# Kernel optimization log

Hardware: AMD Instinct MI355X
Metric: run time of the kernel (lower is better)

Reference implementation:

```python
import jax, jax.numpy as jnp
import numpy as np
import math

B, S, D, H, L, F = 32, 512, 512, 8, 4, 1024
TD = 4 * D  # time embedding dim
DH = D // H
SCALE = 1.0 / math.sqrt(DH)


def _ln(x, g, b):
    m = jnp.mean(x, -1, keepdims=True)
    v = jnp.var(x, -1, keepdims=True)
    return (x - m) * jax.lax.rsqrt(v + 1e-5) * g + b


def setup_inputs() -> dict:
    key = jax.random.key(0)
    ks = jax.random.split(key, 12)
    w = lambda k, shp: jax.random.normal(k, shp, dtype=jnp.float32) * 0.02
    return {
        "x": jax.random.normal(ks[0], (B, S, D), dtype=jnp.float32),
        "time": jax.random.uniform(ks[1], (B,), dtype=jnp.float32) * 1000.0,
        "time_w1": w(ks[2], (TD, D)), "time_b1": jnp.zeros((TD,), jnp.float32),
        "time_w2": w(ks[3], (TD, TD)), "time_b2": jnp.zeros((TD,), jnp.float32),
        "Wq": w(ks[4], (L, D, D)), "bq": jnp.zeros((L, D), jnp.float32),
        "Wk": w(ks[5], (L, D, D)), "bk": jnp.zeros((L, D), jnp.float32),
        "Wv": w(ks[6], (L, D, D)), "bv": jnp.zeros((L, D), jnp.float32),
        "Wo": w(ks[7], (L, D, D)), "bo": jnp.zeros((L, D), jnp.float32),
        "attn_g": jnp.ones((L, D), jnp.float32), "attn_b": jnp.zeros((L, D), jnp.float32),
        "ffn_g": jnp.ones((L, D), jnp.float32), "ffn_b": jnp.zeros((L, D), jnp.float32),
        "W1": w(ks[8], (L, 2 * F, D)), "b1": jnp.zeros((L, 2 * F), jnp.float32),
        "W2": w(ks[9], (L, D, F)), "b2": jnp.zeros((L, D), jnp.float32),
        "Wt": w(ks[10], (L, 4 * F, TD)), "bt": jnp.zeros((L, 4 * F), jnp.float32),
        "head_g": jnp.ones((D,), jnp.float32), "head_b": jnp.zeros((D,), jnp.float32),
        "Wh": w(ks[11], (D, D)), "bh": jnp.zeros((D,), jnp.float32),
    }


def _forward(x, time, time_w1, time_b1, time_w2, time_b2,
             Wq, bq, Wk, bk, Wv, bv, Wo, bo,
             attn_g, attn_b, ffn_g, ffn_b,
             W1, b1, W2, b2, Wt, bt,
             head_g, head_b, Wh, bh):
    Bsz = x.shape[0]
    # --- sinusoidal time embedding + time MLP ---
    half = D // 2
    freqs = jnp.exp(jnp.arange(half, dtype=jnp.float32) * (-math.log(10000.0) / (half - 1)))
    e = time[:, None] * freqs[None, :]
    temb = jnp.concatenate([jnp.sin(e), jnp.cos(e)], axis=-1)  # [B, D]
    temb = jax.nn.gelu(temb @ time_w1.T + time_b1, approximate=False) @ time_w2.T + time_b2  # [B, 4D]
    for i in range(L):
        # attention (prenorm; block 0 skips the norm since first_prenormalization=False)
        h = x if i == 0 else _ln(x, attn_g[i], attn_b[i])
        q = (h @ Wq[i].T + bq[i]).reshape(Bsz, S, H, DH)
        k = (h @ Wk[i].T + bk[i]).reshape(Bsz, S, H, DH)
        v = (h @ Wv[i].T + bv[i]).reshape(Bsz, S, H, DH)
        logits = jnp.einsum('bqhd,bkhd->bhqk', q, k) * SCALE
        probs = jax.nn.softmax(logits, axis=-1)
        o = jnp.einsum('bhqk,bkhd->bqhd', probs, v).reshape(Bsz, S, D)
        x = x + (o @ Wo[i].T + bo[i])
        # FFN with FiLM time conditioning and ReGLU activation
        h = _ln(x, ffn_g[i], ffn_b[i])
        h1 = h @ W1[i].T + b1[i]  # [B, S, 2F]
        tm = jax.nn.silu(temb) @ Wt[i].T + bt[i]  # [B, 4F]
        scale, shift = jnp.split(tm[:, None, :], 2, axis=-1)  # each [B, 1, 2F]
        h1 = h1 * (scale + 1.0) + shift
        a, g = jnp.split(h1, 2, axis=-1)  # ReGLU: a * relu(g)
        x = x + ((a * jax.nn.relu(g)) @ W2[i].T + b2[i])
    # head: last token -> LayerNorm -> ReLU -> Linear
    z = _ln(x[:, -1], head_g, head_b)
    return jax.nn.relu(z) @ Wh.T + bh


def reference(x, time, time_w1, time_b1, time_w2, time_b2,
              Wq, bq, Wk, bk, Wv, bv, Wo, bo,
              attn_g, attn_b, ffn_g, ffn_b,
              W1, b1, W2, b2, Wt, bt,
              head_g, head_b, Wh, bh):
    return _forward(x, time, time_w1, time_b1, time_w2, time_b2,
                    Wq, bq, Wk, bk, Wv, bv, Wo, bo,
                    attn_g, attn_b, ffn_g, ffn_b,
                    W1, b1, W2, b2, Wt, bt,
                    head_g, head_b, Wh, bh)
```

## Files before the change

kernel.cpp:

```cpp
#include <hip/hip_runtime.h>
#include <math.h>

typedef __bf16 bf16_t;
typedef __bf16 bf16x8 __attribute__((ext_vector_type(8)));
typedef float f32x4 __attribute__((ext_vector_type(4)));

__device__ __forceinline__ void gload_lds16(const void* g, void* l) {
    __builtin_amdgcn_global_load_lds(
        (const __attribute__((address_space(1))) void*)g,
        (__attribute__((address_space(3))) void*)l, 16, 0, 0);
}

__global__ void k_f2b(const float* __restrict__ in, bf16_t* __restrict__ out, int n8) {
    int idx = blockIdx.x * 256 + threadIdx.x;
    if (idx >= n8) return;
    const float* p = in + (size_t)idx * 8;
    bf16x8 r;
#pragma unroll
    for (int j = 0; j < 8; j++) r[j] = (bf16_t)p[j];
    *(bf16x8*)(out + (size_t)idx * 8) = r;
}

__global__ void k_f2b_s(const float* __restrict__ in, bf16_t* __restrict__ out,
                        int seg8, int dstride8) {
    int idx = blockIdx.x * 256 + threadIdx.x;
    int seg = idx / seg8, rem = idx - seg * seg8;
    const float* p = in + (size_t)idx * 8;
    bf16x8 r;
#pragma unroll
    for (int j = 0; j < 8; j++) r[j] = (bf16_t)p[j];
    *(bf16x8*)(out + ((size_t)seg * dstride8 + rem) * 8) = r;
}

__global__ void k_time_embed(const float* __restrict__ time, float* __restrict__ temb0) {
    int b = blockIdx.x;
    int j = threadIdx.x;
    float f = __expf((float)j * -0.036118981458730134f);
    float e = time[b] * f;
    temb0[(size_t)b * 512 + j] = sinf(e);
    temb0[(size_t)b * 512 + 256 + j] = cosf(e);
}

template<bool DO_NORM, bool IN32>
__global__ void k_ln(const void* __restrict__ xp, const float* __restrict__ g,
                     const float* __restrict__ b, bf16_t* __restrict__ out) {
    int row = blockIdx.x * 4 + (threadIdx.x >> 6);
    int lane = threadIdx.x & 63;
    float vals[8];
    if (IN32) {
        const float* xr = (const float*)xp + (size_t)row * 512 + lane * 8;
        float4 v0 = *(const float4*)xr;
        float4 v1 = *(const float4*)(xr + 4);
        vals[0] = v0.x; vals[1] = v0.y; vals[2] = v0.z; vals[3] = v0.w;
        vals[4] = v1.x; vals[5] = v1.y; vals[6] = v1.z; vals[7] = v1.w;
    } else {
        bf16x8 xv = *(const bf16x8*)((const bf16_t*)xp + (size_t)row * 512 + lane * 8);
#pragma unroll
        for (int j = 0; j < 8; j++) vals[j] = (float)xv[j];
    }
    bf16x8 r;
    if (DO_NORM) {
        float s = 0.f, sq = 0.f;
#pragma unroll
        for (int j = 0; j < 8; j++) { s += vals[j]; sq += vals[j] * vals[j]; }
#pragma unroll
        for (int m = 1; m < 64; m <<= 1) { s += __shfl_xor(s, m, 64); sq += __shfl_xor(sq, m, 64); }
        float mean = s * (1.0f / 512.0f);
        float var = sq * (1.0f / 512.0f) - mean * mean;
        float rstd = rsqrtf(var + 1e-5f);
        float4 g0 = *(const float4*)(g + lane * 8);
        float4 g1 = *(const float4*)(g + lane * 8 + 4);
        float4 b0 = *(const float4*)(b + lane * 8);
        float4 b1 = *(const float4*)(b + lane * 8 + 4);
        float gs[8] = {g0.x, g0.y, g0.z, g0.w, g1.x, g1.y, g1.z, g1.w};
        float bs[8] = {b0.x, b0.y, b0.z, b0.w, b1.x, b1.y, b1.z, b1.w};
#pragma unroll
        for (int j = 0; j < 8; j++) r[j] = (bf16_t)((vals[j] - mean) * rstd * gs[j] + bs[j]);
    } else {
#pragma unroll
        for (int j = 0; j < 8; j++) r[j] = (bf16_t)vals[j];
    }
    *(bf16x8*)(out + (size_t)row * 512 + lane * 8) = r;
}

__global__ void k_head_prep(const bf16_t* __restrict__ x, const float* __restrict__ g,
                            const float* __restrict__ b, float* __restrict__ z) {
    int row = blockIdx.x * 4 + (threadIdx.x >> 6);
    int lane = threadIdx.x & 63;
    bf16x8 xv = *(const bf16x8*)(x + ((size_t)row * 512 + 511) * 512 + lane * 8);
    float vals[8];
#pragma unroll
    for (int j = 0; j < 8; j++) vals[j] = (float)xv[j];
    float s = 0.f, sq = 0.f;
#pragma unroll
    for (int j = 0; j < 8; j++) { s += vals[j]; sq += vals[j] * vals[j]; }
#pragma unroll
    for (int m = 1; m < 64; m <<= 1) { s += __shfl_xor(s, m, 64); sq += __shfl_xor(sq, m, 64); }
    float mean = s * (1.0f / 512.0f);
    float var = sq * (1.0f / 512.0f) - mean * mean;
    float rstd = rsqrtf(var + 1e-5f);
    float o[8];
#pragma unroll
    for (int j = 0; j < 8; j++) {
        float gv = g[lane * 8 + j], bv = b[lane * 8 + j];
        o[j] = fmaxf((vals[j] - mean) * rstd * gv + bv, 0.0f);
    }
    float* zr = z + (size_t)row * 512 + lane * 8;
    *(float4*)zr = make_float4(o[0], o[1], o[2], o[3]);
    *(float4*)(zr + 4) = make_float4(o[4], o[5], o[6], o[7]);
}

template<int ACT, int K, bool OUTB>
__global__ __launch_bounds__(256, 2)
void k_gemm_tm(const float* __restrict__ A, const float* __restrict__ W,
               const float* __restrict__ bias, void* __restrict__ outp, int N) {
    __shared__ float Asm[32][516];
    const int t = threadIdx.x;
    const int kq = t & 7, rw = (t >> 3) & 7, bh = t >> 6;
    const int n0 = blockIdx.x * 32;
    float acc[4][8] = {};
    for (int k0 = 0; k0 < K; k0 += 512) {
        __syncthreads();
#pragma unroll
        for (int i = 0; i < 16; i++) {
            int fid = t + i * 256;
            int row = fid >> 7, cc = (fid & 127) << 2;
            *(float4*)&Asm[row][cc] = *(const float4*)&A[(size_t)row * K + k0 + cc];
        }
        __syncthreads();
#pragma unroll 4
        for (int j = 0; j < 16; j++) {
            int kk = kq * 4 + j * 32;
            float4 w4[4];
#pragma unroll
            for (int r = 0; r < 4; r++)
                w4[r] = *(const float4*)&W[(size_t)(n0 + rw + r * 8) * K + k0 + kk];
#pragma unroll
            for (int b = 0; b < 8; b++) {
                float4 a4 = *(const float4*)&Asm[bh * 8 + b][kk];
#pragma unroll
                for (int r = 0; r < 4; r++)
                    acc[r][b] += a4.x * w4[r].x + a4.y * w4[r].y + a4.z * w4[r].z + a4.w * w4[r].w;
            }
        }
    }
#pragma unroll
    for (int m = 1; m < 8; m <<= 1)
#pragma unroll
        for (int r = 0; r < 4; r++)
#pragma unroll
            for (int b = 0; b < 8; b++)
                acc[r][b] += __shfl_xor(acc[r][b], m, 64);
    if (kq == 0) {
#pragma unroll
        for (int r = 0; r < 4; r++) {
            int n = n0 + rw + r * 8;
            float bv = bias[n];
#pragma unroll
            for (int b = 0; b < 8; b++) {
                float v = acc[r][b] + bv;
                if (ACT == 1) v = 0.5f * v * (1.0f + erff(v * 0.70710678118654752f));
                if (ACT == 2) v = v / (1.0f + __expf(-v));
                if (OUTB) ((bf16_t*)outp)[(size_t)(bh * 8 + b) * N + n] = (bf16_t)v;
                else      ((float*)outp)[(size_t)(bh * 8 + b) * N + n] = v;
            }
        }
    }
}

__global__ void k_fill_tmt(const float* __restrict__ bt, float* __restrict__ dst) {
    int i = blockIdx.x * 256 + threadIdx.x;
    dst[i] = bt[i >> 5];
}

__global__ void k_silu_t(const float* __restrict__ tmp, bf16_t* __restrict__ t2s_b) {
    int i = blockIdx.x * 256 + threadIdx.x;
    float v = tmp[i];
    v = v / (1.0f + __expf(-v));
    int n = i >> 5, b = i & 31;
    t2s_b[(size_t)b * 2048 + n] = (bf16_t)v;
}

__global__ __launch_bounds__(256, 4)
void k_gemm_wt(const float* __restrict__ Wf, const bf16_t* __restrict__ Bb16,
               float* __restrict__ dst) {
    __shared__ __align__(16) bf16_t Abuf[64 * 64];
    __shared__ __align__(16) bf16_t Bbuf[32 * 64];
    const int tid = threadIdx.x;
    const int m0 = blockIdx.x * 64;
    const int k0 = blockIdx.y * 512;
    const int lane = tid & 63, wave = tid >> 6;
    const int arow = tid >> 2, aseg = tid & 3;
    const int brow = tid >> 3, bseg = tid & 7;
    const int aswz = (arow & 7) << 4;
    const char* Bg = (const char*)Bb16 + (size_t)brow * 4096 + ((bseg * 16) ^ ((brow & 7) << 4));
    char* BbL = (char*)Bbuf + tid * 16;
    const float* Ar0 = Wf + (size_t)(m0 + arow) * 2048 + k0 + aseg * 16;
    f32x4 acc[2] = {};
    for (int kk0 = 0; kk0 < 512; kk0 += 64) {
        float4 a4[4];
#pragma unroll
        for (int i = 0; i < 4; i++) a4[i] = *(const float4*)(Ar0 + kk0 + i * 4);
        __syncthreads();
        gload_lds16(Bg + (size_t)(k0 + kk0) * 2, BbL);
        bf16x8 c0, c1;
#pragma unroll
        for (int i = 0; i < 4; i++) {
            const float* af = (const float*)&a4[i];
#pragma unroll
            for (int j = 0; j < 4; j++) {
                if (i < 2) c0[i * 4 + j] = (bf16_t)af[j];
                else       c1[(i - 2) * 4 + j] = (bf16_t)af[j];
            }
        }
        int base = arow * 128 + aseg * 32;
        *(bf16x8*)((char*)Abuf + (base ^ aswz)) = c0;
        *(bf16x8*)((char*)Abuf + ((base + 16) ^ aswz)) = c1;
        __syncthreads();
#pragma unroll
        for (int kk = 0; kk < 2; kk++) {
            int ar = wave * 16 + (lane & 15);
            bf16x8 af = *(const bf16x8*)((const char*)Abuf + ar * 128 +
                        ((kk * 64 + (lane >> 4) * 16) ^ ((ar & 7) << 4)));
#pragma unroll
            for (int j = 0; j < 2; j++) {
                int br = j * 16 + (lane & 15);
                bf16x8 bfr = *(const bf16x8*)((const char*)Bbuf + br * 128 +
                             ((kk * 64 + (lane >> 4) * 16) ^ ((br & 7) << 4)));
                acc[j] = __builtin_amdgcn_mfma_f32_16x16x32_bf16(af, bfr, acc[j], 0, 0, 0);
            }
        }
    }
#pragma unroll
    for (int j = 0; j < 2; j++)
#pragma unroll
        for (int r = 0; r < 4; r++) {
            int mrow = m0 + wave * 16 + (lane >> 4) * 4 + r;
            atomicAdd(&dst[(size_t)mrow * 32 + j * 16 + (lane & 15)], acc[j][r]);
        }
}

enum { EPI_QKV = 0, EPI_RESID = 1, EPI_FILMGLU = 2 };

template<int EPI, int K, int NBY, int BM, bool RS32>
__global__ __launch_bounds__(BM * 2, 4)
void k_gemm_bt(const bf16_t* __restrict__ A, const bf16_t* __restrict__ W,
               const float* __restrict__ bias, const float* __restrict__ bias2,
               const float* __restrict__ bias3,
               void* __restrict__ out0, const void* __restrict__ rsp, void* __restrict__ out2,
               const float* __restrict__ tm) {
    constexpr int T   = BM * 2;
    constexpr int RPR = BM / 4;
    constexpr int BR  = 512 / BM;
    __shared__ __align__(16) bf16_t Abuf[BM * 64];
    __shared__ __align__(16) bf16_t Bbuf[128 * 64];
    const int tid = threadIdx.x;
    const int cpx = gridDim.x >> 3;
    const int wg = (blockIdx.x & 7) * cpx + (blockIdx.x >> 3);
    const int bx = wg / NBY;
    const int by = wg - bx * NBY;
    const int m0 = bx * BM;
    const int lane = tid & 63;
    const int wid = tid >> 6;
    const int wrM = (wid >> 1) * 64;
    const int wN  = wid & 1;
    const int wc  = wN * 64;

    const int srow = tid >> 3;
    const int goff = ((tid & 7) * 16) ^ ((srow & 7) << 4);
    const char* Ag = (const char*)A;
    const char* Wg = (const char*)W;
    char* AbL = (char*)Abuf + tid * 16;
    char* BbL = (char*)Bbuf + tid * 16;
    int growB[BR];
#pragma unroll
    for (int i = 0; i < BR; i++) {
        int r = srow + i * RPR;
        if (EPI == EPI_FILMGLU) {
            int half = (r >> 5) & 1;
            int base = by * 64 + (r >> 6) * 32 + (r & 31);
            growB[i] = half * 1024 + base;
        } else {
            growB[i] = by * 128 + r;
        }
    }

    f32x4 acc[4][4] = {};
    for (int k0 = 0; k0 < K * 2; k0 += 128) {
        __syncthreads();
#pragma unroll
        for (int i = 0; i < 4; i++)
            gload_lds16(Ag + (size_t)(m0 + srow + i * RPR) * (K * 2) + k0 + goff, AbL + i * (T * 16));
#pragma unroll
        for (int i = 0; i < BR; i++)
            gload_lds16(Wg + (size_t)growB[i] * (K * 2) + k0 + goff, BbL + i * (T * 16));
        __syncthreads();
#pragma unroll
        for (int kk = 0; kk < 2; kk++) {
            bf16x8 af[4], bfr[4];
#pragma unroll
            for (int i = 0; i < 4; i++) {
                int ar = wrM + i * 16 + (lane & 15);
                af[i] = *(const bf16x8*)((const char*)Abuf + ar * 128 +
                         ((kk * 64 + (lane >> 4) * 16) ^ ((ar & 7) << 4)));
                int br = wc + i * 16 + (lane & 15);
                bfr[i] = *(const bf16x8*)((const char*)Bbuf + br * 128 +
                         ((kk * 64 + (lane >> 4) * 16) ^ ((br & 7) << 4)));
            }
#pragma unroll
            for (int i = 0; i < 4; i++)
#pragma unroll
                for (int j = 0; j < 4; j++)
                    acc[i][j] = __builtin_amdgcn_mfma_f32_16x16x32_bf16(af[i], bfr[j], acc[i][j], 0, 0, 0);
        }
    }

    const int b = m0 >> 9;
    if (EPI == EPI_QKV) {
        const int which = by >> 2;
        bf16_t* op = (bf16_t*)(which == 0 ? out0 : which == 1 ? (void*)rsp : out2);
        const float* bp = which == 0 ? bias : which == 1 ? bias2 : bias3;
#pragma unroll
        for (int i = 0; i < 4; i++) {
#pragma unroll
            for (int r = 0; r < 4; r++) {
                int s = (m0 + wrM + i * 16 + (lane >> 4) * 4 + r) & 511;
#pragma unroll
                for (int j = 0; j < 4; j++) {
                    int c = (by & 3) * 128 + wc + j * 16 + (lane & 15);
                    float v = acc[i][j][r] + bp[c];
                    int h = c >> 6, dh = c & 63;
                    op[(((size_t)b * 8 + h) * 512 + s) * 64 + dh] = (bf16_t)v;
                }
            }
        }
    } else if (EPI == EPI_RESID) {
        bf16_t* op = (bf16_t*)out0;
#pragma unroll
        for (int i = 0; i < 4; i++) {
#pragma unroll
            for (int r = 0; r < 4; r++) {
                int row = m0 + wrM + i * 16 + (lane >> 4) * 4 + r;
#pragma unroll
                for (int j = 0; j < 4; j++) {
                    int col = by * 128 + wc + j * 16 + (lane & 15);
                    size_t idx = (size_t)row * 512 + col;
                    float rsv = RS32 ? ((const float*)rsp)[idx] : (float)((const bf16_t*)rsp)[idx];
                    op[idx] = (bf16_t)(rsv + acc[i][j][r] + bias[col]);
                }
            }
        }
    } else {
        bf16_t* op = (bf16_t*)out0;
#pragma unroll
        for (int i = 0; i < 4; i++) {
#pragma unroll
            for (int r = 0; r < 4; r++) {
                int row = m0 + wrM + i * 16 + (lane >> 4) * 4 + r;
#pragma unroll
                for (int jj = 0; jj < 2; jj++) {
                    int colA = by * 64 + wN * 32 + jj * 16 + (lane & 15);
                    float av = acc[i][jj][r] + bias[colA];
                    float gv = acc[i][jj + 2][r] + bias[1024 + colA];
                    float sa = tm[(size_t)colA * 32 + b];
                    float ha = tm[(size_t)(2048 + colA) * 32 + b];
                    float sg = tm[(size_t)(1024 + colA) * 32 + b];
                    float hg = tm[(size_t)(3072 + colA) * 32 + b];
                    av = av * (1.0f + sa) + ha;
                    gv = gv * (1.0f + sg) + hg;
                    op[(size_t)row * 1024 + colA] = (bf16_t)(av * fmaxf(gv, 0.0f));
                }
            }
        }
    }
}

__global__ __launch_bounds__(256, 2)
void k_attn(const bf16_t* __restrict__ q, const bf16_t* __restrict__ k,
            const bf16_t* __restrict__ v, bf16_t* __restrict__ o) {
    __shared__ bf16_t q_lds[2][64][72];
    __shared__ bf16_t k_lds[64][72];
    __shared__ bf16_t vt_lds[64 * 72];
    __shared__ bf16_t p_lds[64][72];
    const int tid = threadIdx.x;
    const int lane = tid & 63;
    const int wave = tid >> 6;
    const int cpx = gridDim.x >> 3;
    const int wg = ((int)blockIdx.x & 7) * cpx + ((int)blockIdx.x >> 3);
    const int bh = wg >> 2;
    const int qt2 = wg & 3;
    const bf16_t* kb = k + (size_t)bh * 512 * 64;
    const bf16_t* vb = v + (size_t)bh * 512 * 64;
    const int sr = tid >> 2;
    const int sc = (tid & 3) * 16;
#pragma unroll
    for (int qi = 0; qi < 2; qi++) {
        const bf16_t* qb = q + ((size_t)bh * 512 + qt2 * 128 + qi * 64) * 64;
        bf16x8 a0 = *(const bf16x8*)(qb + sr * 64 + sc);
        bf16x8 a1 = *(const bf16x8*)(qb + sr * 64 + sc + 8);
        bf16x8 ra, rb;
#pragma unroll
        for (int j = 0; j < 8; j++) {
            ra[j] = (bf16_t)((float)a0[j] * 0.125f);
            rb[j] = (bf16_t)((float)a1[j] * 0.125f);
        }
        *(bf16x8*)&q_lds[qi][sr][sc] = ra;
        *(bf16x8*)&q_lds[qi][sr][sc + 8] = rb;
    }
    bf16x8 kr0, kr1, vr0, vr1;
    {
        const bf16_t* ks = kb + (size_t)sr * 64 + sc;
        const bf16_t* vs = vb + (size_t)sr * 64 + sc;
        kr0 = *(const bf16x8*)ks; kr1 = *(const bf16x8*)(ks + 8);
        vr0 = *(const bf16x8*)vs; vr1 = *(const bf16x8*)(vs + 8);
    }
    float mrow[2][4], lrow[2][4];
    f32x4 oacc[2][4] = {};
#pragma unroll
    for (int qi = 0; qi < 2; qi++)
#pragma unroll
        for (int r = 0; r < 4; r++) { mrow[qi][r] = -1e30f; lrow[qi][r] = 0.f; }
    const int swz0 = ((sc >> 3) & 7) << 4;
    const int swz1 = (((sc + 8) >> 3) & 7) << 4;
    for (int kt = 0; kt < 8; kt++) {
        __syncthreads();
        {
            *(bf16x8*)&k_lds[sr][sc] = kr0;
            *(bf16x8*)&k_lds[sr][sc + 8] = kr1;
            char* vbase = (char*)vt_lds;
            int so0 = (sr * 2) ^ swz0;
            int so1 = (sr * 2) ^ swz1;
#pragma unroll
            for (int j = 0; j < 8; j++) {
                *(bf16_t*)(vbase + (sc + j) * 144 + so0) = vr0[j];
                *(bf16_t*)(vbase + (sc + 8 + j) * 144 + so1) = vr1[j];
            }
        }
        __syncthreads();
        if (kt < 7) {
            const bf16_t* ks = kb + ((size_t)(kt + 1) * 64 + sr) * 64 + sc;
            const bf16_t* vs = vb + ((size_t)(kt + 1) * 64 + sr) * 64 + sc;
            kr0 = *(const bf16x8*)ks; kr1 = *(const bf16x8*)(ks + 8);
            vr0 = *(const bf16x8*)vs; vr1 = *(const bf16x8*)(vs + 8);
        }
#pragma unroll
        for (int qi = 0; qi < 2; qi++) {
            f32x4 sacc[4] = {};
#pragma unroll
            for (int kk = 0; kk < 2; kk++) {
                bf16x8 aq = *(const bf16x8*)&q_lds[qi][wave * 16 + (lane & 15)][kk * 32 + (lane >> 4) * 8];
#pragma unroll
                for (int c = 0; c < 4; c++) {
                    bf16x8 bk8 = *(const bf16x8*)&k_lds[c * 16 + (lane & 15)][kk * 32 + (lane >> 4) * 8];
                    sacc[c] = __builtin_amdgcn_mfma_f32_16x16x32_bf16(aq, bk8, sacc[c], 0, 0, 0);
                }
            }
#pragma unroll
            for (int r = 0; r < 4; r++) {
                float mx = fmaxf(fmaxf(sacc[0][r], sacc[1][r]), fmaxf(sacc[2][r], sacc[3][r]));
#pragma unroll
                for (int m = 1; m < 16; m <<= 1) mx = fmaxf(mx, __shfl_xor(mx, m, 64));
                float newm = fmaxf(mrow[qi][r], mx);
                float fsc = __expf(mrow[qi][r] - newm);
                mrow[qi][r] = newm;
                float p0 = __expf(sacc[0][r] - newm);
                float p1 = __expf(sacc[1][r] - newm);
                float p2 = __expf(sacc[2][r] - newm);
                float p3 = __expf(sacc[3][r] - newm);
                float ps = p0 + p1 + p2 + p3;
#pragma unroll
                for (int m = 1; m < 16; m <<= 1) ps += __shfl_xor(ps, m, 64);
                lrow[qi][r] = lrow[qi][r] * fsc + ps;
#pragma unroll
                for (int c = 0; c < 4; c++) oacc[qi][c][r] *= fsc;
                int qrow = wave * 16 + (lane >> 4) * 4 + r;
                p_lds[qrow][(lane & 15)] = (bf16_t)p0;
                p_lds[qrow][16 + (lane & 15)] = (bf16_t)p1;
                p_lds[qrow][32 + (lane & 15)] = (bf16_t)p2;
                p_lds[qrow][48 + (lane & 15)] = (bf16_t)p3;
            }
#pragma unroll
            for (int kk = 0; kk < 2; kk++) {
                bf16x8 ap = *(const bf16x8*)&p_lds[wave * 16 + (lane & 15)][kk * 32 + (lane >> 4) * 8];
#pragma unroll
                for (int c = 0; c < 4; c++) {
                    int d0 = c * 16 + (lane & 15);
                    int xo = ((d0 >> 3) & 7) << 4;
                    bf16x8 bv8 = *(const bf16x8*)((const char*)vt_lds + d0 * 144 +
                                  ((kk * 64 + (lane >> 4) * 16) ^ xo));
                    oacc[qi][c] = __builtin_amdgcn_mfma_f32_16x16x32_bf16(ap, bv8, oacc[qi][c], 0, 0, 0);
                }
            }
        }
    }
    const int b = bh >> 3, h = bh & 7;
#pragma unroll
    for (int qi = 0; qi < 2; qi++) {
#pragma unroll
        for (int r = 0; r < 4; r++) {
            int s = qt2 * 128 + qi * 64 + wave * 16 + (lane >> 4) * 4 + r;
            float inv = 1.0f / lrow[qi][r];
#pragma unroll
            for (int c = 0; c < 4; c++) {
                o[((size_t)b * 512 + s) * 512 + h * 64 + c * 16 + (lane & 15)] = (bf16_t)(oacc[qi][c][r] * inv);
            }
        }
    }
}

extern "C" void kernel_launch(void* const* d_in, const int* in_sizes, int n_in,
                              void* d_out, int out_size, void* d_ws, size_t ws_size,
                              hipStream_t stream) {
    const float* x_in   = (const float*)d_in[0];
    const float* time_in= (const float*)d_in[1];
    const float* tw1    = (const float*)d_in[2];
    const float* tb1    = (const float*)d_in[3];
    const float* tw2    = (const float*)d_in[4];
    const float* tb2    = (const float*)d_in[5];
    const float* Wq     = (const float*)d_in[6];
    const float* bq     = (const float*)d_in[7];
    const float* Wk     = (const float*)d_in[8];
    const float* bk     = (const float*)d_in[9];
    const float* Wv     = (const float*)d_in[10];
    const float* bv     = (const float*)d_in[11];
    const float* Wo     = (const float*)d_in[12];
    const float* bo     = (const float*)d_in[13];
    const float* attn_g = (const float*)d_in[14];
    const float* attn_b = (const float*)d_in[15];
    const float* ffn_g  = (const float*)d_in[16];
    const float* ffn_b  = (const float*)d_in[17];
    const float* W1     = (const float*)d_in[18];
    const float* b1     = (const float*)d_in[19];
    const float* W2     = (const float*)d_in[20];
    const float* b2     = (const float*)d_in[21];
    const float* Wt     = (const float*)d_in[22];
    const float* bt     = (const float*)d_in[23];
    const float* head_g = (const float*)d_in[24];
    const float* head_b = (const float*)d_in[25];
    const float* Wh     = (const float*)d_in[26];
    const float* bh     = (const float*)d_in[27];

    size_t off = 0;
    auto alloc = [&](size_t bytes) {
        void* r = (char*)d_ws + off;
        off += (bytes + 255) & ~(size_t)255;
        return r;
    };
    bf16_t* wqkv_b = (bf16_t*)alloc((size_t)4 * 3 * 512 * 512 * 2);
    bf16_t* wo_b   = (bf16_t*)alloc((size_t)4 * 512 * 512 * 2);
    bf16_t* w1_b   = (bf16_t*)alloc((size_t)4 * 2048 * 512 * 2);
    bf16_t* w2_b   = (bf16_t*)alloc((size_t)4 * 512 * 1024 * 2);
    bf16_t* x_ws   = (bf16_t*)alloc((size_t)16384 * 512 * 2);
    bf16_t* h_b    = (bf16_t*)alloc((size_t)16384 * 512 * 2);
    bf16_t* q_b    = (bf16_t*)alloc((size_t)16384 * 512 * 2);
    bf16_t* k_b    = (bf16_t*)alloc((size_t)16384 * 512 * 2);
    bf16_t* v_b    = (bf16_t*)alloc((size_t)16384 * 512 * 2);
    bf16_t* o_b    = (bf16_t*)alloc((size_t)16384 * 512 * 2);
    bf16_t* act_b  = (bf16_t*)alloc((size_t)16384 * 1024 * 2);
    float*  temb0  = (float*)alloc((size_t)32 * 512 * 4);
    bf16_t* t1_b   = (bf16_t*)alloc((size_t)32 * 2048 * 2);
    float*  tmp2   = (float*)alloc((size_t)2048 * 32 * 4);
    bf16_t* t2s_b  = (bf16_t*)alloc((size_t)32 * 2048 * 2);
    float*  tm_t   = (float*)alloc((size_t)16384 * 32 * 4);
    float*  z      = (float*)alloc((size_t)32 * 512 * 4);

    k_f2b_s<<<512, 256, 0, stream>>>(Wq, wqkv_b,          32768, 98304);
    k_f2b_s<<<512, 256, 0, stream>>>(Wk, wqkv_b + 262144, 32768, 98304);
    k_f2b_s<<<512, 256, 0, stream>>>(Wv, wqkv_b + 524288, 32768, 98304);
    k_f2b<<<512, 256, 0, stream>>>(Wo, wo_b, 131072);
    k_f2b<<<2048, 256, 0, stream>>>(W1, w1_b, 524288);
    k_f2b<<<1024, 256, 0, stream>>>(W2, w2_b, 262144);

    k_time_embed<<<32, 256, 0, stream>>>(time_in, temb0);
    k_gemm_tm<1, 512, true><<<64, 256, 0, stream>>>(temb0, tw1, tb1, t1_b, 2048);
    k_fill_tmt<<<256, 256, 0, stream>>>(tb2, tmp2);
    k_gemm_wt<<<dim3(32, 4), 256, 0, stream>>>(tw2, t1_b, tmp2);
    k_silu_t<<<256, 256, 0, stream>>>(tmp2, t2s_b);
    k_fill_tmt<<<2048, 256, 0, stream>>>(bt, tm_t);
    k_gemm_wt<<<dim3(256, 4), 256, 0, stream>>>(Wt, t2s_b, tm_t);

    for (int l = 0; l < 4; l++) {
        if (l == 0)
            k_ln<false, true><<<4096, 256, 0, stream>>>(x_in, nullptr, nullptr, h_b);
        else
            k_ln<true, false><<<4096, 256, 0, stream>>>(x_ws, attn_g + l * 512, attn_b + l * 512, h_b);

        k_gemm_bt<EPI_QKV, 512, 12, 128, false><<<1536, 256, 0, stream>>>(
            h_b, wqkv_b + (size_t)l * 786432,
            bq + l * 512, bk + l * 512, bv + l * 512,
            q_b, k_b, v_b, nullptr);

        k_attn<<<1024, 256, 0, stream>>>(q_b, k_b, v_b, o_b);

        if (l == 0)
            k_gemm_bt<EPI_RESID, 512, 4, 128, true><<<512, 256, 0, stream>>>(
                o_b, wo_b + (size_t)l * 262144,
                bo + l * 512, nullptr, nullptr,
                x_ws, x_in, nullptr, nullptr);
        else
            k_gemm_bt<EPI_RESID, 512, 4, 128, false><<<512, 256, 0, stream>>>(
                o_b, wo_b + (size_t)l * 262144,
                bo + l * 512, nullptr, nullptr,
                x_ws, x_ws, nullptr, nullptr);

        k_ln<true, false><<<4096, 256, 0, stream>>>(x_ws, ffn_g + l * 512, ffn_b + l * 512, h_b);

        k_gemm_bt<EPI_FILMGLU, 512, 16, 128, false><<<2048, 256, 0, stream>>>(
            h_b, w1_b + (size_t)l * 1048576,
            b1 + l * 2048, nullptr, nullptr,
            act_b, nullptr, nullptr, tm_t + (size_t)l * 4096 * 32);

        k_gemm_bt<EPI_RESID, 1024, 4, 128, false><<<512, 256, 0, stream>>>(
            act_b, w2_b + (size_t)l * 524288,
            b2 + l * 512, nullptr, nullptr,
            x_ws, x_ws, nullptr, nullptr);
    }

    k_head_prep<<<8, 256, 0, stream>>>(x_ws, head_g, head_b, z);
    k_gemm_tm<0, 512, false><<<16, 256, 0, stream>>>(z, Wh, bh, (float*)d_out, 512);
}
```

Baseline: 1.075 ms.

## Emit V transposed from QKV GEMM and simplify attention V staging

The QKV projection GEMM now computes the V block with swapped MFMA operands and writes V in a [b,h,dh,s] transposed layout. The attention kernel can then stage V into LDS with vector stores instead of per-element scattered transposing writes. It also folds log2(e) into the Q scale so softmax uses exp2f, raises the occupancy hint to 3 blocks per SM, and adds s_setprio around the MFMA sections. The transposed epilogue writes scattered 2-byte stores along s, which may make the GEMM's store pattern less efficient.

```diff
diff --git a/kernel.cpp b/kernel.cpp
--- a/kernel.cpp
+++ b/kernel.cpp
@@ -265,6 +265,7 @@
     const int wrM = (wid >> 1) * 64;
     const int wN  = wid & 1;
     const int wc  = wN * 64;
+    const bool vtr = (EPI == EPI_QKV) && ((by >> 2) == 2);
 
     const int srow = tid >> 3;
     const int goff = ((tid & 7) * 16) ^ ((srow & 7) << 4);
@@ -307,11 +308,19 @@
                 bfr[i] = *(const bf16x8*)((const char*)Bbuf + br * 128 +
                          ((kk * 64 + (lane >> 4) * 16) ^ ((br & 7) << 4)));
             }
-#pragma unroll
-            for (int i = 0; i < 4; i++)
-#pragma unroll
-                for (int j = 0; j < 4; j++)
-                    acc[i][j] = __builtin_amdgcn_mfma_f32_16x16x32_bf16(af[i], bfr[j], acc[i][j], 0, 0, 0);
+            if (vtr) {
+#pragma unroll
+                for (int i = 0; i < 4; i++)
+#pragma unroll
+                    for (int j = 0; j < 4; j++)
+                        acc[i][j] = __builtin_amdgcn_mfma_f32_16x16x32_bf16(bfr[j], af[i], acc[i][j], 0, 0, 0);
+            } else {
+#pragma unroll
+                for (int i = 0; i < 4; i++)
+#pragma unroll
+                    for (int j = 0; j < 4; j++)
+                        acc[i][j] = __builtin_amdgcn_mfma_f32_16x16x32_bf16(af[i], bfr[j], acc[i][j], 0, 0, 0);
+            }
         }
     }
 
@@ -320,17 +329,33 @@
         const int which = by >> 2;
         bf16_t* op = (bf16_t*)(which == 0 ? out0 : which == 1 ? (void*)rsp : out2);
         const float* bp = which == 0 ? bias : which == 1 ? bias2 : bias3;
-#pragma unroll
-        for (int i = 0; i < 4; i++) {
-#pragma unroll
-            for (int r = 0; r < 4; r++) {
-                int s = (m0 + wrM + i * 16 + (lane >> 4) * 4 + r) & 511;
-#pragma unroll
-                for (int j = 0; j < 4; j++) {
-                    int c = (by & 3) * 128 + wc + j * 16 + (lane & 15);
-                    float v = acc[i][j][r] + bp[c];
-                    int h = c >> 6, dh = c & 63;
-                    op[(((size_t)b * 8 + h) * 512 + s) * 64 + dh] = (bf16_t)v;
+        if (vtr) {
+#pragma unroll
+            for (int i = 0; i < 4; i++) {
+#pragma unroll
+                for (int r = 0; r < 4; r++) {
+#pragma unroll
+                    for (int j = 0; j < 4; j++) {
+                        int c = (by & 3) * 128 + wc + j * 16 + (lane >> 4) * 4 + r;
+                        int s = (m0 + wrM + i * 16 + (lane & 15)) & 511;
+                        float v = acc[i][j][r] + bp[c];
+                        op[(((size_t)b * 8 + (c >> 6)) * 64 + (c & 63)) * 512 + s] = (bf16_t)v;
+                    }
+                }
+            }
+        } else {
+#pragma unroll
+            for (int i = 0; i < 4; i++) {
+#pragma unroll
+                for (int r = 0; r < 4; r++) {
+                    int s = (m0 + wrM + i * 16 + (lane >> 4) * 4 + r) & 511;
+#pragma unroll
+                    for (int j = 0; j < 4; j++) {
+                        int c = (by & 3) * 128 + wc + j * 16 + (lane & 15);
+                        float v = acc[i][j][r] + bp[c];
+                        int h = c >> 6, dh = c & 63;
+                        op[(((size_t)b * 8 + h) * 512 + s) * 64 + dh] = (bf16_t)v;
+                    }
                 }
             }
         }
@@ -375,12 +400,12 @@
     }
 }
 
-__global__ __launch_bounds__(256, 2)
+__global__ __launch_bounds__(256, 3)
 void k_attn(const bf16_t* __restrict__ q, const bf16_t* __restrict__ k,
-            const bf16_t* __restrict__ v, bf16_t* __restrict__ o) {
+            const bf16_t* __restrict__ vt, bf16_t* __restrict__ o) {
     __shared__ bf16_t q_lds[2][64][72];
     __shared__ bf16_t k_lds[64][72];
-    __shared__ bf16_t vt_lds[64 * 72];
+    __shared__ bf16_t vt_lds[64][72];
     __shared__ bf16_t p_lds[64][72];
     const int tid = threadIdx.x;
     const int lane = tid & 63;
@@ -390,9 +415,10 @@
     const int bh = wg >> 2;
     const int qt2 = wg & 3;
     const bf16_t* kb = k + (size_t)bh * 512 * 64;
-    const bf16_t* vb = v + (size_t)bh * 512 * 64;
+    const bf16_t* vb = vt + (size_t)bh * 64 * 512;
     const int sr = tid >> 2;
     const int sc = (tid & 3) * 16;
+    const float QS = 0.125f * 1.44269504088896340736f;
 #pragma unroll
     for (int qi = 0; qi < 2; qi++) {
         const bf16_t* qb = q + ((size_t)bh * 512 + qt2 * 128 + qi * 64) * 64;
@@ -401,8 +427,8 @@
         bf16x8 ra, rb;
 #pragma unroll
         for (int j = 0; j < 8; j++) {
-            ra[j] = (bf16_t)((float)a0[j] * 0.125f);
-            rb[j] = (bf16_t)((float)a1[j] * 0.125f);
+            ra[j] = (bf16_t)((float)a0[j] * QS);
+            rb[j] = (bf16_t)((float)a1[j] * QS);
         }
         *(bf16x8*)&q_lds[qi][sr][sc] = ra;
         *(bf16x8*)&q_lds[qi][sr][sc + 8] = rb;
@@ -410,7 +436,7 @@
     bf16x8 kr0, kr1, vr0, vr1;
     {
         const bf16_t* ks = kb + (size_t)sr * 64 + sc;
-        const bf16_t* vs = vb + (size_t)sr * 64 + sc;
+        const bf16_t* vs = vb + (size_t)sr * 512 + sc;
         kr0 = *(const bf16x8*)ks; kr1 = *(const bf16x8*)(ks + 8);
         vr0 = *(const bf16x8*)vs; vr1 = *(const bf16x8*)(vs + 8);
     }
@@ -420,32 +446,25 @@
     for (int qi = 0; qi < 2; qi++)
 #pragma unroll
         for (int r = 0; r < 4; r++) { mrow[qi][r] = -1e30f; lrow[qi][r] = 0.f; }
-    const int swz0 = ((sc >> 3) & 7) << 4;
-    const int swz1 = (((sc + 8) >> 3) & 7) << 4;
     for (int kt = 0; kt < 8; kt++) {
         __syncthreads();
         {
             *(bf16x8*)&k_lds[sr][sc] = kr0;
             *(bf16x8*)&k_lds[sr][sc + 8] = kr1;
-            char* vbase = (char*)vt_lds;
-            int so0 = (sr * 2) ^ swz0;
-            int so1 = (sr * 2) ^ swz1;
-#pragma unroll
-            for (int j = 0; j < 8; j++) {
-                *(bf16_t*)(vbase + (sc + j) * 144 + so0) = vr0[j];
-                *(bf16_t*)(vbase + (sc + 8 + j) * 144 + so1) = vr1[j];
-            }
+            *(bf16x8*)&vt_lds[sr][sc] = vr0;
+            *(bf16x8*)&vt_lds[sr][sc + 8] = vr1;
         }
         __syncthreads();
         if (kt < 7) {
             const bf16_t* ks = kb + ((size_t)(kt + 1) * 64 + sr) * 64 + sc;
-            const bf16_t* vs = vb + ((size_t)(kt + 1) * 64 + sr) * 64 + sc;
+            const bf16_t* vs = vb + (size_t)sr * 512 + (kt + 1) * 64 + sc;
             kr0 = *(const bf16x8*)ks; kr1 = *(const bf16x8*)(ks + 8);
             vr0 = *(const bf16x8*)vs; vr1 = *(const bf16x8*)(vs + 8);
         }
 #pragma unroll
         for (int qi = 0; qi < 2; qi++) {
             f32x4 sacc[4] = {};
+            __builtin_amdgcn_s_setprio(1);
 #pragma unroll
             for (int kk = 0; kk < 2; kk++) {
                 bf16x8 aq = *(const bf16x8*)&q_lds[qi][wave * 16 + (lane & 15)][kk * 32 + (lane >> 4) * 8];
@@ -455,18 +474,19 @@
                     sacc[c] = __builtin_amdgcn_mfma_f32_16x16x32_bf16(aq, bk8, sacc[c], 0, 0, 0);
                 }
             }
+            __builtin_amdgcn_s_setprio(0);
 #pragma unroll
             for (int r = 0; r < 4; r++) {
                 float mx = fmaxf(fmaxf(sacc[0][r], sacc[1][r]), fmaxf(sacc[2][r], sacc[3][r]));
 #pragma unroll
                 for (int m = 1; m < 16; m <<= 1) mx = fmaxf(mx, __shfl_xor(mx, m, 64));
                 float newm = fmaxf(mrow[qi][r], mx);
-                float fsc = __expf(mrow[qi][r] - newm);
+                float fsc = exp2f(mrow[qi][r] - newm);
                 mrow[qi][r] = newm;
-                float p0 = __expf(sacc[0][r] - newm);
-                float p1 = __expf(sacc[1][r] - newm);
-                float p2 = __expf(sacc[2][r] - newm);
-                float p3 = __expf(sacc[3][r] - newm);
+                float p0 = exp2f(sacc[0][r] - newm);
+                float p1 = exp2f(sacc[1][r] - newm);
+                float p2 = exp2f(sacc[2][r] - newm);
+                float p3 = exp2f(sacc[3][r] - newm);
                 float ps = p0 + p1 + p2 + p3;
 #pragma unroll
                 for (int m = 1; m < 16; m <<= 1) ps += __shfl_xor(ps, m, 64);
@@ -479,18 +499,17 @@
                 p_lds[qrow][32 + (lane & 15)] = (bf16_t)p2;
                 p_lds[qrow][48 + (lane & 15)] = (bf16_t)p3;
             }
+            __builtin_amdgcn_s_setprio(1);
 #pragma unroll
             for (int kk = 0; kk < 2; kk++) {
                 bf16x8 ap = *(const bf16x8*)&p_lds[wave * 16 + (lane & 15)][kk * 32 + (lane >> 4) * 8];
 #pragma unroll
                 for (int c = 0; c < 4; c++) {
-                    int d0 = c * 16 + (lane & 15);
-                    int xo = ((d0 >> 3) & 7) << 4;
-                    bf16x8 bv8 = *(const bf16x8*)((const char*)vt_lds + d0 * 144 +
-                                  ((kk * 64 + (lane >> 4) * 16) ^ xo));
+                    bf16x8 bv8 = *(const bf16x8*)&vt_lds[c * 16 + (lane & 15)][kk * 32 + (lane >> 4) * 8];
                     oacc[qi][c] = __builtin_amdgcn_mfma_f32_16x16x32_bf16(ap, bv8, oacc[qi][c], 0, 0, 0);
                 }
             }
+            __builtin_amdgcn_s_setprio(0);
         }
     }
     const int b = bh >> 3, h = bh & 7;
```

New measurement: 1.952 ms. +81.6%, slower.
